# Performance work log

Measured on AMD Instinct MI355X. Metric: run time of the kernel, lower is better.

The kernel has to match this reference:

```python
import jax, jax.numpy as jnp
import numpy as np

B = 128          # graphs
NPG = 512        # nodes per graph
N = B * NPG      # total nodes
DEG = 8
E = N * DEG      # total edges (intra-graph)
D = 100          # num_feature_dim / num_node_labels
HID = 128        # config.hidden
HEADS = 8
F1 = 20          # per-head dim of first GATConv in each GATNet
RATIO = 0.5
K = int(np.ceil(RATIO * NPG))  # nodes kept per graph by SAGPooling
NEG_SLOPE = 0.2


def setup_inputs() -> dict:
    key = jax.random.key(0)
    ks = jax.random.split(key, 24)
    x = jax.random.randint(ks[0], (N,), 0, D)
    # intra-graph random edges: local ids in [0, NPG) + graph offset
    src_l = jax.random.randint(ks[1], (B, NPG * DEG), 0, NPG)
    dst_l = jax.random.randint(ks[2], (B, NPG * DEG), 0, NPG)
    off = (jnp.arange(B) * NPG)[:, None]
    edge_index = jnp.stack([(src_l + off).ravel(), (dst_l + off).ravel()])
    batch = jnp.repeat(jnp.arange(B), NPG)

    def lin(k, fan_in, fan_out):
        return jax.random.normal(k, (fan_in, fan_out), jnp.float32) / np.sqrt(fan_in)

    def att(k, h, f):
        return jax.random.normal(k, (h, f), jnp.float32) * 0.1

    p = {
        # GATNet A (conv1): GATConv(D, 20, heads=8) then GATConv(160, HID, heads=1)
        "W_a1": lin(ks[3], D, HEADS * F1), "asrc_a1": att(ks[4], HEADS, F1),
        "adst_a1": att(ks[5], HEADS, F1), "b_a1": jnp.zeros((HEADS * F1,), jnp.float32),
        "W_a2": lin(ks[6], HEADS * F1, HID), "asrc_a2": att(ks[7], 1, HID),
        "adst_a2": att(ks[8], 1, HID), "b_a2": jnp.zeros((HID,), jnp.float32),
        # GATNet B (conv4): GATConv(HID, 20, heads=8) then GATConv(160, HID, heads=1)
        "W_b1": lin(ks[9], HID, HEADS * F1), "asrc_b1": att(ks[10], HEADS, F1),
        "adst_b1": att(ks[11], HEADS, F1), "b_b1": jnp.zeros((HEADS * F1,), jnp.float32),
        "W_b2": lin(ks[12], HEADS * F1, HID), "asrc_b2": att(ks[13], 1, HID),
        "adst_b2": att(ks[14], 1, HID), "b_b2": jnp.zeros((HID,), jnp.float32),
        # SAGPooling GraphConv(HID, 1)
        "w_rel": lin(ks[15], HID, 1), "w_root": lin(ks[16], HID, 1),
        "b_pool": jnp.zeros((1,), jnp.float32),
    }
    return {"x": x, "edge_index": edge_index, "batch": batch, **p}


def _gat_conv(h, src, dst, W, asrc, adst, b):
    """PyG GATConv (with self-loops already included in src/dst)."""
    Hh, Ff = asrc.shape
    z = (h @ W).reshape(N, Hh, Ff)                       # [N,H,F]
    es = jnp.sum(z * asrc, axis=-1)                      # [N,H] source logits
    ed = jnp.sum(z * adst, axis=-1)                      # [N,H] dest logits
    e = jax.nn.leaky_relu(es[src] + ed[dst], NEG_SLOPE)  # [E',H]
    m = jax.ops.segment_max(e, dst, num_segments=N)
    m = jnp.where(jnp.isfinite(m), m, 0.0)
    ex = jnp.exp(e - m[dst])
    den = jax.ops.segment_sum(ex, dst, num_segments=N)
    alpha = ex / (den[dst] + 1e-16)
    out = jax.ops.segment_sum(z[src] * alpha[:, :, None], dst, num_segments=N)
    return out.reshape(N, Hh * Ff) + b


def reference(x, edge_index, batch,
              W_a1, asrc_a1, adst_a1, b_a1, W_a2, asrc_a2, adst_a2, b_a2,
              W_b1, asrc_b1, adst_b1, b_b1, W_b2, asrc_b2, adst_b2, b_b2,
              w_rel, w_root, b_pool):
    src, dst = edge_index[0], edge_index[1]
    loops = jnp.arange(N)
    src_sl = jnp.concatenate([src, loops])  # GATConv adds self loops
    dst_sl = jnp.concatenate([dst, loops])

    h = jax.nn.one_hot(x, D, dtype=jnp.float32)
    # GATNet A: conv1 -> relu -> conv2 ; outer relu (dropout is eval no-op)
    h = jax.nn.relu(_gat_conv(h, src_sl, dst_sl, W_a1, asrc_a1, adst_a1, b_a1))
    h = _gat_conv(h, src_sl, dst_sl, W_a2, asrc_a2, adst_a2, b_a2)
    h = jax.nn.relu(h)
    # GATNet B
    h = jax.nn.relu(_gat_conv(h, src_sl, dst_sl, W_b1, asrc_b1, adst_b1, b_b1))
    h = _gat_conv(h, src_sl, dst_sl, W_b2, asrc_b2, adst_b2, b_b2)
    h = jax.nn.relu(h)

    # SAGPooling: GraphConv(HID,1) score (no self loops), tanh, per-graph top-k
    nbr = jax.ops.segment_sum(h[src], dst, num_segments=N)
    score = jnp.tanh(nbr @ w_rel + h @ w_root + b_pool).ravel()   # [N]
    sv, si = jax.lax.top_k(score.reshape(B, NPG), K)              # [B,K]
    perm = (si + (jnp.arange(B) * NPG)[:, None]).ravel()          # global node ids
    x_sel = h[perm] * sv.ravel()[:, None]                         # [B*K, HID]
    pooled = jnp.max(x_sel.reshape(B, K, HID), axis=1)            # global_max_pool
    batch_out = jnp.repeat(jnp.arange(B), K)
    return (pooled, perm, sv.ravel(), batch_out)
```

## Files before the change

kernel.cpp:

```cpp
#include <hip/hip_runtime.h>
#include <math.h>

#define N_NODES 65536
#define NPG     512
#define NGRAPH  128
#define E_EDGES 524288
#define MAXDEG  64
#define NHEADS  8
#define F1      20
#define HID     128
#define D160    160
#define KSEL    256

typedef unsigned short ushort_t;
typedef unsigned int   uint_t;
typedef unsigned long long u64;
typedef __attribute__((ext_vector_type(8))) short short8;
typedef __attribute__((ext_vector_type(4))) float f32x4;

__device__ __forceinline__ float lrelu(float x){ return x > 0.f ? x : 0.2f*x; }
__device__ __forceinline__ ushort_t f2bf(float f){
    uint_t u = __float_as_uint(f);
    return (ushort_t)((u + 0x7FFFu + ((u >> 16) & 1u)) >> 16);
}
__device__ __forceinline__ float bf2f(ushort_t u){ return __uint_as_float(((uint_t)u) << 16); }
__device__ __forceinline__ float bflo(uint_t v){ return __uint_as_float(v << 16); }
__device__ __forceinline__ float bfhi(uint_t v){ return __uint_as_float(v & 0xFFFF0000u); }
__device__ __forceinline__ int xswz(int bid, int nblocks){
    return (bid & 7) * (nblocks >> 3) + (bid >> 3);
}
__device__ __forceinline__ float rdlanef(float v, int i){
    return __uint_as_float((uint_t)__builtin_amdgcn_readlane(__float_as_int(v), i));
}

__device__ __forceinline__ u64 comp_make(float s, int idx){
    uint_t u = __float_as_uint(s);
    u ^= (u & 0x80000000u) ? 0xFFFFFFFFu : 0x80000000u;
    return ((u64)u << 32) | (u64)(511 - idx);
}
__device__ __forceinline__ float comp_score(u64 c){
    uint_t u = (uint_t)(c >> 32);
    u ^= (u & 0x80000000u) ? 0x80000000u : 0xFFFFFFFFu;
    return __uint_as_float(u);
}
__device__ __forceinline__ int comp_idx(u64 c){ return 511 - (int)(c & 0x1FFu); }
__device__ __forceinline__ u64 shfl_xor_u64(u64 x, int m){
    uint_t lo = __shfl_xor((uint_t)x, m);
    uint_t hi = __shfl_xor((uint_t)(x >> 32), m);
    return ((u64)hi << 32) | lo;
}

__global__ void k_build_ell(const int* __restrict__ src, const int* __restrict__ dst,
                            int* __restrict__ deg, int* __restrict__ ell){
    int blk = xswz(blockIdx.x, E_EDGES/256);
    int e = blk*blockDim.x + threadIdx.x;
    int d = dst[e];
    int p = atomicAdd(&deg[d], 1);
    if(p < MAXDEG) ell[d*MAXDEG + p] = src[e];
}

__global__ void k_a1_z(const int* __restrict__ x, const float* __restrict__ W,
                       const float* __restrict__ asrc, const float* __restrict__ adst,
                       ushort_t* __restrict__ z8, float* __restrict__ es8, float* __restrict__ ed8){
    int blk = xswz(blockIdx.x, N_NODES*NHEADS/256);
    int t = blk*blockDim.x + threadIdx.x;
    int n = t >> 3, h = t & 7;
    int lbl = x[n];
    const float* wrow = W + lbl*D160 + h*F1;
    const float* as = asrc + h*F1;
    const float* ad = adst + h*F1;
    uint_t* zr = (uint_t*)(z8 + (size_t)n*D160 + h*F1);
    float es = 0.f, ed = 0.f;
    #pragma unroll
    for(int f=0; f<10; ++f){
        float v0 = wrow[2*f], v1 = wrow[2*f+1];
        zr[f] = (uint_t)f2bf(v0) | ((uint_t)f2bf(v1) << 16);
        es += v0*as[2*f] + v1*as[2*f+1];
        ed += v0*ad[2*f] + v1*ad[2*f+1];
    }
    es8[t] = es; ed8[t] = ed;
}

__global__ void k_esed8(const ushort_t* __restrict__ z8, const float* __restrict__ asrc,
                        const float* __restrict__ adst,
                        float* __restrict__ es8, float* __restrict__ ed8){
    int blk = xswz(blockIdx.x, N_NODES*NHEADS/256);
    int t = blk*blockDim.x + threadIdx.x;
    int n = t >> 3, h = t & 7;
    const uint_t* zr = (const uint_t*)(z8 + (size_t)n*D160 + h*F1);
    const float* as = asrc + h*F1;
    const float* ad = adst + h*F1;
    float es = 0.f, ed = 0.f;
    #pragma unroll
    for(int f=0; f<10; ++f){
        uint_t v = zr[f];
        float v0 = bflo(v), v1 = bfhi(v);
        es += v0*as[2*f] + v1*as[2*f+1];
        ed += v0*ad[2*f] + v1*ad[2*f+1];
    }
    es8[t] = es; ed8[t] = ed;
}

__global__ void k_attn8(const int* __restrict__ deg, const int* __restrict__ ell,
                        const ushort_t* __restrict__ z8, const float* __restrict__ es8,
                        const float* __restrict__ ed8, const float* __restrict__ bias,
                        ushort_t* __restrict__ out){
    int blk = xswz(blockIdx.x, N_NODES*NHEADS/256);
    int t = blk*blockDim.x + threadIdx.x;
    int n = t >> 3, h = t & 7;
    int dg = deg[n]; if(dg > MAXDEG) dg = MAXDEG;
    float edn = ed8[t];
    float eself = lrelu(es8[t] + edn);
    const int* el = ell + n*MAXDEG;
    float m = eself;
    {
        int i = 0;
        for(; i+2 <= dg; i += 2){
            int sa = el[i], sb = el[i+1];
            float ea = es8[sa*NHEADS + h], eb = es8[sb*NHEADS + h];
            m = fmaxf(m, fmaxf(lrelu(ea + edn), lrelu(eb + edn)));
        }
        if(i < dg){
            float ea = es8[el[i]*NHEADS + h];
            m = fmaxf(m, lrelu(ea + edn));
        }
    }
    float w = expf(eself - m);
    float den = w;
    float acc[F1];
    const uint_t* zn = (const uint_t*)(z8 + (size_t)n*D160 + h*F1);
    #pragma unroll
    for(int f=0; f<10; ++f){
        uint_t v = zn[f];
        acc[2*f]   = w*bflo(v);
        acc[2*f+1] = w*bfhi(v);
    }
    {
        int i = 0;
        for(; i+2 <= dg; i += 2){
            int sa = el[i], sb = el[i+1];
            float ea = es8[sa*NHEADS + h], eb = es8[sb*NHEADS + h];
            const uint_t* za = (const uint_t*)(z8 + (size_t)sa*D160 + h*F1);
            const uint_t* zb = (const uint_t*)(z8 + (size_t)sb*D160 + h*F1);
            float wa = expf(lrelu(ea + edn) - m);
            float wb = expf(lrelu(eb + edn) - m);
            den += wa + wb;
            #pragma unroll
            for(int f=0; f<10; ++f){
                uint_t va = za[f], vb = zb[f];
                acc[2*f]   += wa*bflo(va) + wb*bflo(vb);
                acc[2*f+1] += wa*bfhi(va) + wb*bfhi(vb);
            }
        }
        if(i < dg){
            int sa = el[i];
            float ea = es8[sa*NHEADS + h];
            const uint_t* za = (const uint_t*)(z8 + (size_t)sa*D160 + h*F1);
            float wa = expf(lrelu(ea + edn) - m);
            den += wa;
            #pragma unroll
            for(int f=0; f<10; ++f){
                uint_t va = za[f];
                acc[2*f]   += wa*bflo(va);
                acc[2*f+1] += wa*bfhi(va);
            }
        }
    }
    float inv = 1.f/(den + 1e-16f);
    uint_t* o = (uint_t*)(out + (size_t)n*D160 + h*F1);
    const float* bb = bias + h*F1;
    #pragma unroll
    for(int f=0; f<10; ++f){
        float v0 = fmaxf(acc[2*f]*inv   + bb[2*f],   0.f);
        float v1 = fmaxf(acc[2*f+1]*inv + bb[2*f+1], 0.f);
        o[f] = (uint_t)f2bf(v0) | ((uint_t)f2bf(v1) << 16);
    }
}

template<int IN, int OUT, bool DOT>
__global__ __launch_bounds__(256) void k_gemm_mfma(const ushort_t* __restrict__ A,
                                                   const float* __restrict__ W,
                                                   ushort_t* __restrict__ C,
                                                   const float* __restrict__ va,
                                                   const float* __restrict__ vb,
                                                   float* __restrict__ oa,
                                                   float* __restrict__ ob){
    constexpr int NT = OUT/16;
    constexpr int KS = IN/32;
    constexpr int LDW = IN + 8;
    __shared__ __align__(16) ushort_t Wt[OUT*LDW];
    int tid = threadIdx.x;
    for(int i = tid; i < IN*OUT; i += 256){
        int k = i / OUT, n = i - k*OUT;
        Wt[n*LDW + k] = f2bf(W[i]);
    }
    __syncthreads();
    int blk = xswz(blockIdx.x, N_NODES/64);
    int wave = tid >> 6, lane = tid & 63;
    int col16 = lane & 15;
    int kq = (lane >> 4) * 8;
    int row = blk*64 + wave*16 + col16;
    const ushort_t* Ar = A + (size_t)row*IN + kq;
    f32x4 acc[NT];
    #pragma unroll
    for(int c=0;c<NT;++c) acc[c] = (f32x4){0.f,0.f,0.f,0.f};
    #pragma unroll
    for(int ks=0; ks<KS; ++ks){
        short8 af = *reinterpret_cast<const short8*>(Ar + ks*32);
        #pragma unroll
        for(int c=0;c<NT;++c){
            short8 bf = *reinterpret_cast<const short8*>(&Wt[(c*16 + col16)*LDW + ks*32 + kq]);
            acc[c] = __builtin_amdgcn_mfma_f32_16x16x32_bf16(af, bf, acc[c], 0, 0, 0);
        }
    }
    int rbase = blk*64 + wave*16 + (lane >> 4)*4;
    #pragma unroll
    for(int c=0;c<NT;++c){
        #pragma unroll
        for(int r=0;r<4;++r){
            C[(size_t)(rbase + r)*OUT + c*16 + col16] = f2bf(acc[c][r]);
        }
    }
    if(DOT){
        float pa[4] = {0,0,0,0}, pb[4] = {0,0,0,0};
        #pragma unroll
        for(int c=0;c<NT;++c){
            float a = va[c*16 + col16];
            float b = vb[c*16 + col16];
            #pragma unroll
            for(int r=0;r<4;++r){ pa[r] += acc[c][r]*a; pb[r] += acc[c][r]*b; }
        }
        #pragma unroll
        for(int o=1;o<16;o<<=1){
            #pragma unroll
            for(int r=0;r<4;++r){ pa[r] += __shfl_xor(pa[r], o); pb[r] += __shfl_xor(pb[r], o); }
        }
        if(col16 == 0){
            #pragma unroll
            for(int r=0;r<4;++r){ oa[rbase + r] = pa[r]; ob[rbase + r] = pb[r]; }
        }
    }
}

template<typename OutT, bool DOT>
__global__ void k_attn1(const int* __restrict__ deg, const int* __restrict__ ell,
                        const ushort_t* __restrict__ Z, const float* __restrict__ es,
                        const float* __restrict__ ed, const float* __restrict__ bias,
                        OutT* __restrict__ out,
                        const float* __restrict__ wa, const float* __restrict__ wb,
                        float* __restrict__ oa, float* __restrict__ ob){
    int blk = xswz(blockIdx.x, N_NODES/4);
    int gt = blk*blockDim.x + threadIdx.x;
    int n = gt >> 6;
    int l = threadIdx.x & 63;
    int dg = deg[n]; if(dg > MAXDEG) dg = MAXDEG;
    float edn = ed[n];
    float eself = lrelu(es[n] + edn);
    int s_l = 0; float e_l = -1e30f;
    if(l < dg){ s_l = ell[n*MAXDEG + l]; e_l = lrelu(es[s_l] + edn); }
    float m = fmaxf(e_l, eself);
    for(int o=32;o>0;o>>=1) m = fmaxf(m, __shfl_xor(m,o));
    float w_l = (l < dg) ? expf(e_l - m) : 0.f;
    float den = w_l;
    for(int o=32;o>0;o>>=1) den += __shfl_xor(den,o);
    float wself = expf(eself - m);
    den += wself;
    const uint_t* Zu = (const uint_t*)Z;
    uint_t zn = Zu[(size_t)n*64 + l];
    float acc0 = wself*bflo(zn);
    float acc1 = wself*bfhi(zn);
    int i = 0;
    for(; i+4 <= dg; i += 4){
        int s0 = __builtin_amdgcn_readlane(s_l, i);
        int s1 = __builtin_amdgcn_readlane(s_l, i+1);
        int s2 = __builtin_amdgcn_readlane(s_l, i+2);
        int s3 = __builtin_amdgcn_readlane(s_l, i+3);
        uint_t z0 = Zu[(size_t)s0*64 + l];
        uint_t z1 = Zu[(size_t)s1*64 + l];
        uint_t z2 = Zu[(size_t)s2*64 + l];
        uint_t z3 = Zu[(size_t)s3*64 + l];
        float w0 = rdlanef(w_l, i);
        float w1 = rdlanef(w_l, i+1);
        float w2 = rdlanef(w_l, i+2);
        float w3 = rdlanef(w_l, i+3);
        acc0 += w0*bflo(z0) + w1*bflo(z1);
        acc1 += w0*bfhi(z0) + w1*bfhi(z1);
        acc0 += w2*bflo(z2) + w3*bflo(z3);
        acc1 += w2*bfhi(z2) + w3*bfhi(z3);
    }
    for(; i < dg; ++i){
        int s0 = __builtin_amdgcn_readlane(s_l, i);
        float w0 = rdlanef(w_l, i);
        uint_t z0 = Zu[(size_t)s0*64 + l];
        acc0 += w0*bflo(z0);
        acc1 += w0*bfhi(z0);
    }
    float inv = 1.f/(den + 1e-16f);
    float2 bb = ((const float2*)bias)[l];
    float r0 = fmaxf(acc0*inv + bb.x, 0.f);
    float r1 = fmaxf(acc1*inv + bb.y, 0.f);
    if(sizeof(OutT) == 2){
        ((uint_t*)out)[(size_t)n*64 + l] = (uint_t)f2bf(r0) | ((uint_t)f2bf(r1) << 16);
    } else {
        float2 rv; rv.x = r0; rv.y = r1;
        ((float2*)out)[(size_t)n*64 + l] = rv;
    }
    if(DOT){
        float2 a2 = ((const float2*)wa)[l];
        float2 b2 = ((const float2*)wb)[l];
        float pa = r0*a2.x + r1*a2.y;
        float pb = r0*b2.x + r1*b2.y;
        for(int o=32;o>0;o>>=1){ pa += __shfl_xor(pa,o); pb += __shfl_xor(pb,o); }
        if(l==0){ oa[n] = pa; ob[n] = pb; }
    }
}

__global__ void k_score(const int* __restrict__ deg, const int* __restrict__ ell,
                        const float* __restrict__ yrel, const float* __restrict__ rroot,
                        const float* __restrict__ bpool, float* __restrict__ score){
    int blk = xswz(blockIdx.x, N_NODES/256);
    int n = blk*blockDim.x + threadIdx.x;
    int dg = deg[n]; if(dg > MAXDEG) dg = MAXDEG;
    float s = rroot[n] + bpool[0];
    const int* el = ell + n*MAXDEG;
    int i = 0;
    for(; i+4 <= dg; i += 4){
        float y0 = yrel[el[i]],   y1 = yrel[el[i+1]];
        float y2 = yrel[el[i+2]], y3 = yrel[el[i+3]];
        s += (y0 + y1) + (y2 + y3);
    }
    for(; i < dg; ++i) s += yrel[el[i]];
    score[n] = tanhf(s);
}

__global__ __launch_bounds__(512) void k_topk_pool(const float* __restrict__ score,
                                                   const float* __restrict__ H,
                                                   float* __restrict__ pooled,
                                                   float* __restrict__ perm_f,
                                                   float* __restrict__ sv,
                                                   float* __restrict__ batch_f){
    __shared__ int   sidx[KSEL];
    __shared__ float sval[KSEL];
    __shared__ float pmax[512];
    int g = xswz(blockIdx.x, NGRAPH);
    int base = g*NPG;
    int t = threadIdx.x;
    if(t < 64){
        int l = t;
        u64 v[8];
        #pragma unroll
        for(int r=0;r<8;++r){
            int i = r*64 + l;
            v[r] = comp_make(score[base + i], i);
        }
        #pragma unroll
        for(int kk=1; kk<=9; ++kk){
            int k = 1 << kk;
            #pragma unroll
            for(int jj=kk-1; jj>=0; --jj){
                int j = 1 << jj;
                if(j < 64){
                    bool lower = (l & j) == 0;
                    #pragma unroll
                    for(int r=0;r<8;++r){
                        int i = r*64 + l;
                        u64 p = shfl_xor_u64(v[r], j);
                        bool desc = (i & k) == 0;
                        u64 mx = v[r] > p ? v[r] : p;
                        u64 mn = v[r] > p ? p : v[r];
                        v[r] = (lower == desc) ? mx : mn;
                    }
                } else {
                    int jr = j >> 6;
                    #pragma unroll
                    for(int r=0;r<8;++r){
                        if((r & jr) == 0){
                            int rp = r | jr;
                            int i = r*64 + l;
                            bool desc = (i & k) == 0;
                            u64 a = v[r], b = v[rp];
                            u64 mx = a > b ? a : b;
                            u64 mn = a > b ? b : a;
                            v[r]  = desc ? mx : mn;
                            v[rp] = desc ? mn : mx;
                        }
                    }
                }
            }
        }
        #pragma unroll
        for(int r=0;r<4;++r){
            int i = r*64 + l;
            int idx = comp_idx(v[r]);
            float s = comp_score(v[r]);
            perm_f[g*KSEL + i]  = (float)(base + idx);
            sv[g*KSEL + i]      = s;
            batch_f[g*KSEL + i] = (float)g;
            sidx[i] = idx; sval[i] = s;
        }
    }
    __syncthreads();
    int c = t & 127, kc = t >> 7;
    float mx = -1e30f;
    for(int kk = kc*64; kk < kc*64 + 64; ++kk){
        mx = fmaxf(mx, H[(size_t)(base + sidx[kk])*HID + c] * sval[kk]);
    }
    pmax[t] = mx;
    __syncthreads();
    if(t < HID){
        pooled[g*HID + t] = fmaxf(fmaxf(pmax[t], pmax[t+128]),
                                  fmaxf(pmax[t+256], pmax[t+384]));
    }
}

extern "C" void kernel_launch(void* const* d_in, const int* in_sizes, int n_in,
                              void* d_out, int out_size, void* d_ws, size_t ws_size,
                              hipStream_t stream) {
    const int*   x       = (const int*)  d_in[0];
    const int*   eidx    = (const int*)  d_in[1];
    const float* W_a1    = (const float*)d_in[3];
    const float* asrc_a1 = (const float*)d_in[4];
    const float* adst_a1 = (const float*)d_in[5];
    const float* b_a1    = (const float*)d_in[6];
    const float* W_a2    = (const float*)d_in[7];
    const float* asrc_a2 = (const float*)d_in[8];
    const float* adst_a2 = (const float*)d_in[9];
    const float* b_a2    = (const float*)d_in[10];
    const float* W_b1    = (const float*)d_in[11];
    const float* asrc_b1 = (const float*)d_in[12];
    const float* adst_b1 = (const float*)d_in[13];
    const float* b_b1    = (const float*)d_in[14];
    const float* W_b2    = (const float*)d_in[15];
    const float* asrc_b2 = (const float*)d_in[16];
    const float* adst_b2 = (const float*)d_in[17];
    const float* b_b2    = (const float*)d_in[18];
    const float* w_rel   = (const float*)d_in[19];
    const float* w_root  = (const float*)d_in[20];
    const float* b_pool  = (const float*)d_in[21];

    const int* e_src = eidx;
    const int* e_dst = eidx + E_EDGES;

    char* ws = (char*)d_ws;
    size_t off = 0;
    auto alloc = [&](size_t bytes)->char*{
        char* p = ws + off;
        off += (bytes + 255) & ~(size_t)255;
        return p;
    };
    int*      deg   = (int*)     alloc((size_t)N_NODES*4);
    int*      ell   = (int*)     alloc((size_t)N_NODES*MAXDEG*4);
    ushort_t* z8    = (ushort_t*)alloc((size_t)N_NODES*D160*2);
    ushort_t* h8    = (ushort_t*)alloc((size_t)N_NODES*D160*2);
    ushort_t* zc    = (ushort_t*)alloc((size_t)N_NODES*HID*2);
    ushort_t* hmid  = (ushort_t*)alloc((size_t)N_NODES*HID*2);
    float*    hfin  = (float*)   alloc((size_t)N_NODES*HID*4);
    float*    es8   = (float*)   alloc((size_t)N_NODES*NHEADS*4);
    float*    ed8   = (float*)   alloc((size_t)N_NODES*NHEADS*4);
    float*    es1   = (float*)   alloc((size_t)N_NODES*4);
    float*    ed1   = (float*)   alloc((size_t)N_NODES*4);
    float*    yrel  = (float*)   alloc((size_t)N_NODES*4);
    float*    rroot = (float*)   alloc((size_t)N_NODES*4);
    float*    score = (float*)   alloc((size_t)N_NODES*4);
    (void)ws_size; (void)n_in; (void)in_sizes; (void)out_size;

    float* out      = (float*)d_out;
    float* pooled   = out;
    float* perm_f   = out + NGRAPH*HID;
    float* sv       = perm_f + NGRAPH*KSEL;
    float* batch_f  = sv + NGRAPH*KSEL;

    hipMemsetAsync(deg, 0, (size_t)N_NODES*4, stream);
    k_build_ell<<<E_EDGES/256, 256, 0, stream>>>(e_src, e_dst, deg, ell);

    k_a1_z<<<N_NODES*NHEADS/256, 256, 0, stream>>>(x, W_a1, asrc_a1, adst_a1, z8, es8, ed8);
    k_attn8<<<N_NODES*NHEADS/256, 256, 0, stream>>>(deg, ell, z8, es8, ed8, b_a1, h8);

    k_gemm_mfma<D160, HID, true><<<N_NODES/64, 256, 0, stream>>>(h8, W_a2, zc, asrc_a2, adst_a2, es1, ed1);
    k_attn1<ushort_t, false><<<N_NODES/4, 256, 0, stream>>>(deg, ell, zc, es1, ed1, b_a2, hmid,
                                                            nullptr, nullptr, nullptr, nullptr);

    k_gemm_mfma<HID, D160, false><<<N_NODES/64, 256, 0, stream>>>(hmid, W_b1, z8, nullptr, nullptr, nullptr, nullptr);
    k_esed8<<<N_NODES*NHEADS/256, 256, 0, stream>>>(z8, asrc_b1, adst_b1, es8, ed8);
    k_attn8<<<N_NODES*NHEADS/256, 256, 0, stream>>>(deg, ell, z8, es8, ed8, b_b1, h8);

    k_gemm_mfma<D160, HID, true><<<N_NODES/64, 256, 0, stream>>>(h8, W_b2, zc, asrc_b2, adst_b2, es1, ed1);
    k_attn1<float, true><<<N_NODES/4, 256, 0, stream>>>(deg, ell, zc, es1, ed1, b_b2, hfin,
                                                        w_rel, w_root, yrel, rroot);

    k_score<<<N_NODES/256, 256, 0, stream>>>(deg, ell, yrel, rroot, b_pool, score);
    k_topk_pool<<<NGRAPH, NPG, 0, stream>>>(score, hfin, pooled, perm_f, sv, batch_f);
}
```

Baseline: 254.7 us.

## Fold attention projections into GEMM, widen attn8 to two heads per thread, fuse score

Three changes. First, the separate k_esed8 pass is removed: the per-head attention source and destination projections are precomputed as W·a columns and appended as an extra 16-column MFMA tile in a dedicated b1 GEMM. Second, k_attn8 now handles two heads per thread with uint4 and float2 vector loads, halving the thread count and widening memory accesses. Third, the SAGPooling score computation is fused into the top-k kernel through shared memory, removing one launch and a global round trip, at the cost of more register pressure in attn8 and slightly different bf16 rounding for es/ed.

New measurement: 264.2 us. 3.7% more time.

```diff
diff --git a/kernel.cpp b/kernel.cpp
--- a/kernel.cpp
+++ b/kernel.cpp
@@ -81,100 +81,129 @@
     es8[t] = es; ed8[t] = ed;
 }
 
-__global__ void k_esed8(const ushort_t* __restrict__ z8, const float* __restrict__ asrc,
-                        const float* __restrict__ adst,
-                        float* __restrict__ es8, float* __restrict__ ed8){
-    int blk = xswz(blockIdx.x, N_NODES*NHEADS/256);
-    int t = blk*blockDim.x + threadIdx.x;
-    int n = t >> 3, h = t & 7;
-    const uint_t* zr = (const uint_t*)(z8 + (size_t)n*D160 + h*F1);
-    const float* as = asrc + h*F1;
-    const float* ad = adst + h*F1;
-    float es = 0.f, ed = 0.f;
-    #pragma unroll
-    for(int f=0; f<10; ++f){
-        uint_t v = zr[f];
-        float v0 = bflo(v), v1 = bfhi(v);
-        es += v0*as[2*f] + v1*as[2*f+1];
-        ed += v0*ad[2*f] + v1*ad[2*f+1];
-    }
-    es8[t] = es; ed8[t] = ed;
-}
-
 __global__ void k_attn8(const int* __restrict__ deg, const int* __restrict__ ell,
                         const ushort_t* __restrict__ z8, const float* __restrict__ es8,
                         const float* __restrict__ ed8, const float* __restrict__ bias,
                         ushort_t* __restrict__ out){
-    int blk = xswz(blockIdx.x, N_NODES*NHEADS/256);
-    int t = blk*blockDim.x + threadIdx.x;
-    int n = t >> 3, h = t & 7;
+    int blk = xswz(blockIdx.x, N_NODES*4/256);
+    int p = blk*blockDim.x + threadIdx.x;
+    int n = p >> 2, hp = p & 3;
     int dg = deg[n]; if(dg > MAXDEG) dg = MAXDEG;
-    float edn = ed8[t];
-    float eself = lrelu(es8[t] + edn);
+    float2 edn = *(const float2*)(ed8 + (size_t)n*8 + hp*2);
+    float2 esn = *(const float2*)(es8 + (size_t)n*8 + hp*2);
+    float ese0 = lrelu(esn.x + edn.x), ese1 = lrelu(esn.y + edn.y);
     const int* el = ell + n*MAXDEG;
-    float m = eself;
+    float m0 = ese0, m1 = ese1;
     {
         int i = 0;
         for(; i+2 <= dg; i += 2){
             int sa = el[i], sb = el[i+1];
-            float ea = es8[sa*NHEADS + h], eb = es8[sb*NHEADS + h];
-            m = fmaxf(m, fmaxf(lrelu(ea + edn), lrelu(eb + edn)));
+            float2 ea = *(const float2*)(es8 + (size_t)sa*8 + hp*2);
+            float2 eb = *(const float2*)(es8 + (size_t)sb*8 + hp*2);
+            m0 = fmaxf(m0, fmaxf(lrelu(ea.x + edn.x), lrelu(eb.x + edn.x)));
+            m1 = fmaxf(m1, fmaxf(lrelu(ea.y + edn.y), lrelu(eb.y + edn.y)));
         }
         if(i < dg){
-            float ea = es8[el[i]*NHEADS + h];
-            m = fmaxf(m, lrelu(ea + edn));
-        }
-    }
-    float w = expf(eself - m);
-    float den = w;
-    float acc[F1];
-    const uint_t* zn = (const uint_t*)(z8 + (size_t)n*D160 + h*F1);
-    #pragma unroll
-    for(int f=0; f<10; ++f){
-        uint_t v = zn[f];
-        acc[2*f]   = w*bflo(v);
-        acc[2*f+1] = w*bfhi(v);
+            float2 ea = *(const float2*)(es8 + (size_t)el[i]*8 + hp*2);
+            m0 = fmaxf(m0, lrelu(ea.x + edn.x));
+            m1 = fmaxf(m1, lrelu(ea.y + edn.y));
+        }
+    }
+    float w0 = expf(ese0 - m0), w1 = expf(ese1 - m1);
+    float den0 = w0, den1 = w1;
+    float acc[40];
+    {
+        const uint4* zn = (const uint4*)(z8 + (size_t)n*D160 + hp*40);
+        #pragma unroll
+        for(int q=0; q<5; ++q){
+            uint4 v = zn[q];
+            const uint_t* vu = (const uint_t*)&v;
+            #pragma unroll
+            for(int r=0; r<4; ++r){
+                int ch = q*8 + r*2;
+                float w = (ch < 20) ? w0 : w1;
+                float wN = (ch+1 < 20) ? w0 : w1;
+                acc[ch]   = w *bflo(vu[r]);
+                acc[ch+1] = wN*bfhi(vu[r]);
+            }
+        }
     }
     {
         int i = 0;
         for(; i+2 <= dg; i += 2){
             int sa = el[i], sb = el[i+1];
-            float ea = es8[sa*NHEADS + h], eb = es8[sb*NHEADS + h];
-            const uint_t* za = (const uint_t*)(z8 + (size_t)sa*D160 + h*F1);
-            const uint_t* zb = (const uint_t*)(z8 + (size_t)sb*D160 + h*F1);
-            float wa = expf(lrelu(ea + edn) - m);
-            float wb = expf(lrelu(eb + edn) - m);
-            den += wa + wb;
-            #pragma unroll
-            for(int f=0; f<10; ++f){
-                uint_t va = za[f], vb = zb[f];
-                acc[2*f]   += wa*bflo(va) + wb*bflo(vb);
-                acc[2*f+1] += wa*bfhi(va) + wb*bfhi(vb);
+            float2 ea = *(const float2*)(es8 + (size_t)sa*8 + hp*2);
+            float2 eb = *(const float2*)(es8 + (size_t)sb*8 + hp*2);
+            const uint4* za = (const uint4*)(z8 + (size_t)sa*D160 + hp*40);
+            const uint4* zb = (const uint4*)(z8 + (size_t)sb*D160 + hp*40);
+            uint4 va[5], vb[5];
+            #pragma unroll
+            for(int q=0;q<5;++q){ va[q] = za[q]; vb[q] = zb[q]; }
+            float wa0 = expf(lrelu(ea.x + edn.x) - m0);
+            float wa1 = expf(lrelu(ea.y + edn.y) - m1);
+            float wb0 = expf(lrelu(eb.x + edn.x) - m0);
+            float wb1 = expf(lrelu(eb.y + edn.y) - m1);
+            den0 += wa0 + wb0; den1 += wa1 + wb1;
+            #pragma unroll
+            for(int q=0; q<5; ++q){
+                const uint_t* au = (const uint_t*)&va[q];
+                const uint_t* bu = (const uint_t*)&vb[q];
+                #pragma unroll
+                for(int r=0; r<4; ++r){
+                    int ch = q*8 + r*2;
+                    float wA  = (ch   < 20) ? wa0 : wa1;
+                    float wB  = (ch   < 20) ? wb0 : wb1;
+                    float wAn = (ch+1 < 20) ? wa0 : wa1;
+                    float wBn = (ch+1 < 20) ? wb0 : wb1;
+                    acc[ch]   += wA *bflo(au[r]) + wB *bflo(bu[r]);
+                    acc[ch+1] += wAn*bfhi(au[r]) + wBn*bfhi(bu[r]);
+                }
             }
         }
         if(i < dg){
             int sa = el[i];
-            float ea = es8[sa*NHEADS + h];
-            const uint_t* za = (const uint_t*)(z8 + (size_t)sa*D160 + h*F1);
-            float wa = expf(lrelu(ea + edn) - m);
-            den += wa;
-            #pragma unroll
-            for(int f=0; f<10; ++f){
-                uint_t va = za[f];
-                acc[2*f]   += wa*bflo(va);
-                acc[2*f+1] += wa*bfhi(va);
+            float2 ea = *(const float2*)(es8 + (size_t)sa*8 + hp*2);
+            const uint4* za = (const uint4*)(z8 + (size_t)sa*D160 + hp*40);
+            uint4 va[5];
+            #pragma unroll
+            for(int q=0;q<5;++q) va[q] = za[q];
+            float wa0 = expf(lrelu(ea.x + edn.x) - m0);
+            float wa1 = expf(lrelu(ea.y + edn.y) - m1);
+            den0 += wa0; den1 += wa1;
+            #pragma unroll
+            for(int q=0; q<5; ++q){
+                const uint_t* au = (const uint_t*)&va[q];
+                #pragma unroll
+                for(int r=0; r<4; ++r){
+                    int ch = q*8 + r*2;
+                    float wA  = (ch   < 20) ? wa0 : wa1;
+                    float wAn = (ch+1 < 20) ? wa0 : wa1;
+                    acc[ch]   += wA *bflo(au[r]);
+                    acc[ch+1] += wAn*bfhi(au[r]);
+                }
             }
         }
     }
-    float inv = 1.f/(den + 1e-16f);
-    uint_t* o = (uint_t*)(out + (size_t)n*D160 + h*F1);
-    const float* bb = bias + h*F1;
-    #pragma unroll
-    for(int f=0; f<10; ++f){
-        float v0 = fmaxf(acc[2*f]*inv   + bb[2*f],   0.f);
-        float v1 = fmaxf(acc[2*f+1]*inv + bb[2*f+1], 0.f);
-        o[f] = (uint_t)f2bf(v0) | ((uint_t)f2bf(v1) << 16);
-    }
+    float inv0 = 1.f/(den0 + 1e-16f);
+    float inv1 = 1.f/(den1 + 1e-16f);
+    const float* bb = bias + hp*40;
+    uint4 ov[5];
+    #pragma unroll
+    for(int q=0; q<5; ++q){
+        uint_t* ou = (uint_t*)&ov[q];
+        #pragma unroll
+        for(int r=0; r<4; ++r){
+            int ch = q*8 + r*2;
+            float i0 = (ch   < 20) ? inv0 : inv1;
+            float i1 = (ch+1 < 20) ? inv0 : inv1;
+            float v0 = fmaxf(acc[ch]*i0   + bb[ch],   0.f);
+            float v1 = fmaxf(acc[ch+1]*i1 + bb[ch+1], 0.f);
+            ou[r] = (uint_t)f2bf(v0) | ((uint_t)f2bf(v1) << 16);
+        }
+    }
+    uint4* o = (uint4*)(out + (size_t)n*D160 + hp*40);
+    #pragma unroll
+    for(int q=0; q<5; ++q) o[q] = ov[q];
 }
 
 template<int IN, int OUT, bool DOT>
@@ -239,6 +268,64 @@
             #pragma unroll
             for(int r=0;r<4;++r){ oa[rbase + r] = pa[r]; ob[rbase + r] = pb[r]; }
         }
+    }
+}
+
+__global__ __launch_bounds__(256) void k_gemm_b1(const ushort_t* __restrict__ A,
+                                                 const float* __restrict__ W,
+                                                 const float* __restrict__ asrc,
+                                                 const float* __restrict__ adst,
+                                                 ushort_t* __restrict__ C,
+                                                 float* __restrict__ es8,
+                                                 float* __restrict__ ed8){
+    constexpr int IN = HID, OUTW = D160, NT = 11, KS = IN/32, LDW = IN + 8;
+    __shared__ __align__(16) ushort_t Wt[(OUTW+16)*LDW];
+    int tid = threadIdx.x;
+    for(int i = tid; i < IN*OUTW; i += 256){
+        int k = i / OUTW, n = i - k*OUTW;
+        Wt[n*LDW + k] = f2bf(W[i]);
+    }
+    for(int i = tid; i < IN*16; i += 256){
+        int k = i >> 4, j = i & 15;
+        const float* av = (j < 8 ? asrc : adst) + (j & 7)*F1;
+        const float* wr = W + k*OUTW + (j & 7)*F1;
+        float s = 0.f;
+        #pragma unroll
+        for(int f=0; f<F1; ++f) s += wr[f]*av[f];
+        Wt[(OUTW + j)*LDW + k] = f2bf(s);
+    }
+    __syncthreads();
+    int blk = xswz(blockIdx.x, N_NODES/64);
+    int wave = tid >> 6, lane = tid & 63;
+    int col16 = lane & 15;
+    int kq = (lane >> 4) * 8;
+    int row = blk*64 + wave*16 + col16;
+    const ushort_t* Ar = A + (size_t)row*IN + kq;
+    f32x4 acc[NT];
+    #pragma unroll
+    for(int c=0;c<NT;++c) acc[c] = (f32x4){0.f,0.f,0.f,0.f};
+    #pragma unroll
+    for(int ks=0; ks<KS; ++ks){
+        short8 af = *reinterpret_cast<const short8*>(Ar + ks*32);
+        #pragma unroll
+        for(int c=0;c<NT;++c){
+            short8 bf = *reinterpret_cast<const short8*>(&Wt[(c*16 + col16)*LDW + ks*32 + kq]);
+            acc[c] = __builtin_amdgcn_mfma_f32_16x16x32_bf16(af, bf, acc[c], 0, 0, 0);
+        }
+    }
+    int rbase = blk*64 + wave*16 + (lane >> 4)*4;
+    #pragma unroll
+    for(int c=0;c<10;++c){
+        #pragma unroll
+        for(int r=0;r<4;++r){
+            C[(size_t)(rbase + r)*OUTW + c*16 + col16] = f2bf(acc[c][r]);
+        }
+    }
+    #pragma unroll
+    for(int r=0;r<4;++r){
+        float v = acc[10][r];
+        if(col16 < 8) es8[(size_t)(rbase + r)*8 + col16] = v;
+        else          ed8[(size_t)(rbase + r)*8 + (col16 - 8)] = v;
     }
 }
 
@@ -315,43 +402,45 @@
     }
 }
 
-__global__ void k_score(const int* __restrict__ deg, const int* __restrict__ ell,
-                        const float* __restrict__ yrel, const float* __restrict__ rroot,
-                        const float* __restrict__ bpool, float* __restrict__ score){
-    int blk = xswz(blockIdx.x, N_NODES/256);
-    int n = blk*blockDim.x + threadIdx.x;
-    int dg = deg[n]; if(dg > MAXDEG) dg = MAXDEG;
-    float s = rroot[n] + bpool[0];
-    const int* el = ell + n*MAXDEG;
-    int i = 0;
-    for(; i+4 <= dg; i += 4){
-        float y0 = yrel[el[i]],   y1 = yrel[el[i+1]];
-        float y2 = yrel[el[i+2]], y3 = yrel[el[i+3]];
-        s += (y0 + y1) + (y2 + y3);
-    }
-    for(; i < dg; ++i) s += yrel[el[i]];
-    score[n] = tanhf(s);
-}
-
-__global__ __launch_bounds__(512) void k_topk_pool(const float* __restrict__ score,
+__global__ __launch_bounds__(512) void k_topk_pool(const int* __restrict__ deg,
+                                                   const int* __restrict__ ell,
+                                                   const float* __restrict__ yrel,
+                                                   const float* __restrict__ rroot,
+                                                   const float* __restrict__ bpool,
                                                    const float* __restrict__ H,
                                                    float* __restrict__ pooled,
                                                    float* __restrict__ perm_f,
                                                    float* __restrict__ sv,
                                                    float* __restrict__ batch_f){
+    __shared__ float ssc[NPG];
     __shared__ int   sidx[KSEL];
     __shared__ float sval[KSEL];
     __shared__ float pmax[512];
     int g = xswz(blockIdx.x, NGRAPH);
     int base = g*NPG;
     int t = threadIdx.x;
+    {
+        int n = base + t;
+        int dg = deg[n]; if(dg > MAXDEG) dg = MAXDEG;
+        float s = rroot[n] + bpool[0];
+        const int* el = ell + n*MAXDEG;
+        int i = 0;
+        for(; i+4 <= dg; i += 4){
+            float y0 = yrel[el[i]],   y1 = yrel[el[i+1]];
+            float y2 = yrel[el[i+2]], y3 = yrel[el[i+3]];
+            s += (y0 + y1) + (y2 + y3);
+        }
+        for(; i < dg; ++i) s += yrel[el[i]];
+        ssc[t] = tanhf(s);
+    }
+    __syncthreads();
     if(t < 64){
         int l = t;
         u64 v[8];
         #pragma unroll
         for(int r=0;r<8;++r){
             int i = r*64 + l;
-            v[r] = comp_make(score[base + i], i);
+            v[r] = comp_make(ssc[i], i);
         }
         #pragma unroll
         for(int kk=1; kk<=9; ++kk){
@@ -461,7 +550,6 @@
     float*    ed1   = (float*)   alloc((size_t)N_NODES*4);
     float*    yrel  = (float*)   alloc((size_t)N_NODES*4);
     float*    rroot = (float*)   alloc((size_t)N_NODES*4);
-    float*    score = (float*)   alloc((size_t)N_NODES*4);
     (void)ws_size; (void)n_in; (void)in_sizes; (void)out_size;
 
     float* out      = (float*)d_out;
@@ -474,20 +562,19 @@
     k_build_ell<<<E_EDGES/256, 256, 0, stream>>>(e_src, e_dst, deg, ell);
 
     k_a1_z<<<N_NODES*NHEADS/256, 256, 0, stream>>>(x, W_a1, asrc_a1, adst_a1, z8, es8, ed8);
-    k_attn8<<<N_NODES*NHEADS/256, 256, 0, stream>>>(deg, ell, z8, es8, ed8, b_a1, h8);
+    k_attn8<<<N_NODES*4/256, 256, 0, stream>>>(deg, ell, z8, es8, ed8, b_a1, h8);
 
     k_gemm_mfma<D160, HID, true><<<N_NODES/64, 256, 0, stream>>>(h8, W_a2, zc, asrc_a2, adst_a2, es1, ed1);
     k_attn1<ushort_t, false><<<N_NODES/4, 256, 0, stream>>>(deg, ell, zc, es1, ed1, b_a2, hmid,
                                                             nullptr, nullptr, nullptr, nullptr);
 
-    k_gemm_mfma<HID, D160, false><<<N_NODES/64, 256, 0, stream>>>(hmid, W_b1, z8, nullptr, nullptr, nullptr, nullptr);
-    k_esed8<<<N_NODES*NHEADS/256, 256, 0, stream>>>(z8, asrc_b1, adst_b1, es8, ed8);
-    k_attn8<<<N_NODES*NHEADS/256, 256, 0, stream>>>(deg, ell, z8, es8, ed8, b_b1, h8);
+    k_gemm_b1<<<N_NODES/64, 256, 0, stream>>>(hmid, W_b1, asrc_b1, adst_b1, z8, es8, ed8);
+    k_attn8<<<N_NODES*4/256, 256, 0, stream>>>(deg, ell, z8, es8, ed8, b_b1, h8);
 
     k_gemm_mfma<D160, HID, true><<<N_NODES/64, 256, 0, stream>>>(h8, W_b2, zc, asrc_b2, adst_b2, es1, ed1);
     k_attn1<float, true><<<N_NODES/4, 256, 0, stream>>>(deg, ell, zc, es1, ed1, b_b2, hfin,
                                                         w_rel, w_root, yrel, rroot);
 
-    k_score<<<N_NODES/256, 256, 0, stream>>>(deg, ell, yrel, rroot, b_pool, score);
-    k_topk_pool<<<NGRAPH, NPG, 0, stream>>>(score, hfin, pooled, perm_f, sv, batch_f);
-}
+    k_topk_pool<<<NGRAPH, NPG, 0, stream>>>(deg, ell, yrel, rroot, b_pool, hfin,
+                                            pooled, perm_f, sv, batch_f);
+}
```
